# Optimization experiments

Hardware: AMD Instinct MI355X
Metric: run time of the kernel (lower is better)

Reference implementation:

```python
import jax, jax.numpy as jnp
import numpy as np
from jax import lax

B, C, T, D, H, W = 1, 8, 8, 24, 48, 48
KT = 3  # temporal kernel taps (module's time loop == valid forward conv, stride 1, pad 0)
KS = 3  # spatial kernel size
S = 2   # spatial stride of the transposed conv
P = 1   # spatial padding of the transposed conv


def setup_inputs() -> dict:
    key = jax.random.key(0)
    kx, kw = jax.random.split(key)
    x = jax.random.normal(kx, (B, C, T, D, H, W), dtype=jnp.float32)
    # torch layout (out_channels, in_channels, kT, kD, kH, kW); the module assigns the
    # slice weight[:, :, i] directly as ConvTranspose3d.weight, so at runtime dim0 acts
    # as the transpose-conv INPUT-channel dim (works because in_ch == out_ch).
    fan_in = C * KT * KS ** 3
    bound = float(1.0 / np.sqrt(fan_in))
    weight = jax.random.uniform(kw, (C, C, KT, KS, KS, KS), dtype=jnp.float32,
                                minval=-bound, maxval=bound)
    return {"x": x, "weight": weight}


def _convT3d(x5, wt):
    # x5: [N, Cin, D, H, W]; wt: ConvTranspose3d weight laid out [Cin, Cout, kD, kH, kW].
    # Transposed conv == forward conv with spatially flipped kernel, swapped I/O dims,
    # lhs dilation = stride, per-side padding = dil*(k-1) - p.
    rhs = jnp.flip(wt, axis=(2, 3, 4)).transpose(1, 0, 2, 3, 4)  # [Cout, Cin, k, k, k]
    pad = KS - 1 - P
    return lax.conv_general_dilated(
        x5, rhs,
        window_strides=(1, 1, 1),
        padding=[(pad, pad)] * 3,
        lhs_dilation=(S, S, S),
        dimension_numbers=("NCDHW", "OIDHW", "NCDHW"))


def reference(x, weight):
    b, c, t = x.shape[:3]
    t_o = t - (KT - 1)  # temporal valid forward conv: out[f] = sum_i conv_i(x[f + i])
    # fold time into batch so each temporal tap is a single big 3D conv
    xr = x.transpose(0, 2, 1, 3, 4, 5).reshape(b * t, c, *x.shape[3:])
    out = None
    for i in range(KT):  # small fixed loop over kernel taps
        y = _convT3d(xr, weight[:, :, i])                 # [b*t, C, Do, Ho, Wo]
        y = y.reshape(b, t, *y.shape[1:])[:, i:i + t_o]   # frames x[f+i] -> out[f]
        out = y if out is None else out + y
    return out.transpose(0, 2, 1, 3, 4, 5)  # [B, C, t_o, Do, Ho, Wo]
```

## Files before the change

kernel.cpp:

```cpp
#include <hip/hip_runtime.h>


typedef float  f32x4  __attribute__((ext_vector_type(4)));
typedef float  f4a    __attribute__((ext_vector_type(4)));
typedef short  bf16x8 __attribute__((ext_vector_type(8)));
typedef unsigned int u32;
typedef u32    u32x2  __attribute__((ext_vector_type(2)));
typedef u32    u32x4  __attribute__((ext_vector_type(4)));

namespace {
constexpr int T_ = 8, D_ = 24, H_ = 48, W_ = 48;
constexpr int TO = 6, DO_ = 47, HO = 95, WO = 95;
constexpr int XCS = T_ * D_ * H_ * W_;
constexpr int XFS = D_ * H_ * W_;
constexpr int XDS = H_ * W_;
constexpr long OCS = (long)TO * DO_ * HO * WO;
constexpr int OFS = DO_ * HO * WO;
constexpr int ODS = HO * WO;

constexpr int AG[4] = {24, 12, 12, 8};
constexpr int AOFF[4] = {0, 3072, 4608, 6144};
constexpr int NRSTR = 242;

__global__ __launch_bounds__(256) void pack_kernel(const float* __restrict__ w,
                                                   unsigned short* __restrict__ A) {
  const int tid = blockIdx.x * 256 + threadIdx.x;
  const int nthr = gridDim.x * 256;
  const int KR[4] = {192, 96, 96, 48};
  for (int c = 0; c < 4; ++c) {
    const int cnt = AG[c] * 128;
    for (int e = tid; e < cnt; e += nthr) {
      const int j = e & 7, r = (e >> 3) & 15, g = e >> 7;
      const int k = g * 8 + j;
      float v = 0.f;
      if (k < KR[c]) {
        int gg = -1, kd = 1, kh = 1;
        const int cc = j & 1;
        if (c == 0)      { gg = g;               kd = ((j >> 1) & 1) ? 2 : 0; kh = ((j >> 2) & 1) ? 0 : 2; }
        else if (c == 1) { gg = 2 * g + (j >> 2); kd = ((j >> 1) & 1) ? 2 : 0; kh = 1; }
        else if (c == 2) { gg = 2 * g + (j >> 2); kd = 1; kh = ((j >> 1) & 1) ? 0 : 2; }
        else             { gg = 4 * g + (j >> 1); kd = 1; kh = 1; }
        if (gg >= 0 && gg < 24) {
          const int ci = gg / 3, i = gg - 3 * (gg / 3);
          const int co = r & 7;
          int kw = (r < 8) ? (cc == 0 ? 1 : -1) : (cc == 0 ? 2 : 0);
          if (kw >= 0) v = w[ci * 648 + co * 81 + i * 27 + kd * 9 + kh * 3 + kw];
        }
      }
      u32 u = __float_as_uint(v);
      u += 0x7FFFu + ((u >> 16) & 1u);
      A[AOFF[c] + e] = (unsigned short)(u >> 16);
    }
  }
}

__device__ __forceinline__ int rowb(int gg, int dl) {
  const int ci = gg / 3;
  return (ci * 5 + (gg - 3 * ci) + dl) * 6;
}

template<int PD, int PH>
__device__ __forceinline__ void wave_body(
    const u32* __restrict__ lds, const unsigned short* __restrict__ A,
    float* __restrict__ out, int f0, int od, int oh, int ihb, int lane)
{
  constexpr int CLS = (PD && PH) ? 0 : PD ? 1 : PH ? 2 : 3;
  constexpr int NSTEP = (CLS == 0) ? 6 : (CLS == 3) ? 2 : 3;
  const int c15 = lane & 15, q = lane >> 4;
  const int th = ((oh + PH) >> 1) - ihb;

  bf16x8 af[NSTEP];
  {
    const unsigned short* Ap = A + AOFF[CLS] + c15 * 8;
    #pragma unroll
    for (int s = 0; s < NSTEP; ++s)
      af[s] = *reinterpret_cast<const bf16x8*>(Ap + (s * 4 + q) * 128);
  }

  f32x4 acc[3][3];
  #pragma unroll
  for (int dl = 0; dl < 3; ++dl)
    #pragma unroll
    for (int b = 0; b < 3; ++b) acc[dl][b] = {0, 0, 0, 0};

  #pragma unroll
  for (int blk = 0; blk < 3; ++blk) {
    const int n = blk * 16 + c15;
    const u32* col = lds + n * NRSTR;
    #pragma unroll
    for (int s = 0; s < NSTEP; ++s) {
      const int G = s * 4 + q;
      #pragma unroll
      for (int dl = 0; dl < 3; ++dl) {
        u32x4 ue;
        if constexpr (CLS == 0) {
          const u32* b = col + rowb(G, dl) + 2 * th - 2;
          const u32x2 lo = *reinterpret_cast<const u32x2*>(b);
          const u32x2 hi = *reinterpret_cast<const u32x2*>(b + 2);
          ue = u32x4{lo.x, lo.y, hi.x, hi.y};
        } else if constexpr (CLS == 1) {
          const u32* b0 = col + rowb(2 * G, dl) + 2 * th;
          const u32* b1 = col + rowb(2 * G + 1, dl) + 2 * th;
          const u32x2 lo = *reinterpret_cast<const u32x2*>(b0);
          const u32x2 hi = *reinterpret_cast<const u32x2*>(b1);
          ue = u32x4{lo.x, lo.y, hi.x, hi.y};
        } else if constexpr (CLS == 2) {
          const int r0 = rowb(2 * G, dl), r1 = rowb(2 * G + 1, dl);
          ue = u32x4{col[r0 + 2 * th - 1], col[r0 + 2 * th + 1],
                     col[r1 + 2 * th - 1], col[r1 + 2 * th + 1]};
        } else {
          #pragma unroll
          for (int d = 0; d < 4; ++d) {
            int gg = 4 * G + d; gg = (gg > 23) ? 23 : gg;
            ue[d] = col[rowb(gg, dl) + 2 * th + 1];
          }
        }
        acc[dl][blk] = __builtin_amdgcn_mfma_f32_16x16x32_bf16(af[s], __builtin_bit_cast(bf16x8, ue), acc[dl][blk], 0, 0, 0);
      }
    }
  }

  const int isO = (q >= 2);
  const int co0 = (q & 1) * 4;
  #pragma unroll
  for (int dl = 0; dl < 3; ++dl) {
    #pragma unroll
    for (int blk = 0; blk < 3; ++blk) {
      const int ow = blk * 32 + 2 * c15 + isO;
      if (ow < 95) {
        const long ob = (long)(f0 + dl) * OFS + (long)od * ODS + (long)oh * HO + ow;
        #pragma unroll
        for (int j = 0; j < 4; ++j)
          out[(long)(co0 + j) * OCS + ob] = acc[dl][blk][j];
      }
    }
  }
}

constexpr int NBLK = 2 * 24 * 24;

__global__ __launch_bounds__(512) void convt4d_kernel(
    const float* __restrict__ x, const unsigned short* __restrict__ A,
    float* __restrict__ out)
{
  __shared__ u32 lds[48 * NRSTR];

  constexpr int qq = NBLK / 8;
  const int bid = blockIdx.x;
  const int L = (bid & 7) * qq + (bid >> 3);
  const int og = L % 24;
  const int rest = L / 24;
  const int odp = rest % 24, fp = rest / 24;
  const int f0 = 3 * fp;

  const int tid = threadIdx.x;
  const int ihb = og * 2;
  const int idp = odp + 1;

  for (int c = tid; c < 240 * 12; c += 512) {
    const int row = c / 12, ch = c % 12;
    const int ggp = row / 6;
    const int rem = row % 6;
    const int t = rem >> 1, e = rem & 1;
    const int ci = ggp / 5, fi = ggp % 5;
    int plane = idp - e; if (plane > 23) plane = 23;
    int ih = ihb + t; if (ih > 47) ih = 47;
    const float* src = x + ci * XCS + (f0 + fi) * XFS + plane * XDS + ih * W_ + ch * 4;
    const f4a v = *reinterpret_cast<const f4a*>(src);
    const float v4 = (ch == 11) ? 0.f : src[4];
    const u32 b0 = __float_as_uint(v.x), b1 = __float_as_uint(v.y);
    const u32 b2 = __float_as_uint(v.z), b3 = __float_as_uint(v.w);
    const u32 b4 = __float_as_uint(v4);
    u32* dst = lds + (4 * ch) * NRSTR + row;
    dst[0 * NRSTR] = __builtin_amdgcn_perm(b1, b0, 0x07060302u);
    dst[1 * NRSTR] = __builtin_amdgcn_perm(b2, b1, 0x07060302u);
    dst[2 * NRSTR] = __builtin_amdgcn_perm(b3, b2, 0x07060302u);
    dst[3 * NRSTR] = __builtin_amdgcn_perm(b4, b3, 0x07060302u);
  }
  __syncthreads();

  const int w = tid >> 6, lane = tid & 63;
  const int half = w >> 2;
  const int od = 2 * odp + half;
  if (od > 46) return;
  int oh = og * 4 + (w & 3);
  if (oh > 94) oh = 93;
  if (half) {
    if (oh & 1) wave_body<1, 1>(lds, A, out, f0, od, oh, ihb, lane);
    else        wave_body<1, 0>(lds, A, out, f0, od, oh, ihb, lane);
  } else {
    if (oh & 1) wave_body<0, 1>(lds, A, out, f0, od, oh, ihb, lane);
    else        wave_body<0, 0>(lds, A, out, f0, od, oh, ihb, lane);
  }
}
}

extern "C" void kernel_launch(void* const* d_in, const int* in_sizes, int n_in,
                              void* d_out, int out_size, void* d_ws, size_t ws_size,
                              hipStream_t stream) {
  const float* x = (const float*)d_in[0];
  const float* w = (const float*)d_in[1];
  float* out = (float*)d_out;
  unsigned short* A = (unsigned short*)d_ws;
  hipLaunchKernelGGL(pack_kernel, dim3(8), dim3(256), 0, stream, w, A);
  hipLaunchKernelGGL(convt4d_kernel, dim3(NBLK), dim3(512), 0, stream, x, A, out);
}
```

Baseline: 32.88 us.

## Stage input tile via direct global-to-LDS loads, pack bf16 pairs at read time

The input staging loop used to load float4 vectors into registers, build bf16 pairs with perm, and write them transposed into a padded LDS layout. It now copies raw fp32 rows straight into LDS with global_load_lds (16-byte per lane) in row-major order. The bf16 pair packing moves into the MFMA operand gather, where each element becomes two LDS reads plus a perm. Staging gets cheaper, but the inner loop does twice as many LDS reads with a different bank pattern. The unpadded layout may also cause bank conflicts.

```diff
diff --git a/kernel.cpp b/kernel.cpp
--- a/kernel.cpp
+++ b/kernel.cpp
@@ -2,10 +2,8 @@
 
 
 typedef float  f32x4  __attribute__((ext_vector_type(4)));
-typedef float  f4a    __attribute__((ext_vector_type(4)));
 typedef short  bf16x8 __attribute__((ext_vector_type(8)));
 typedef unsigned int u32;
-typedef u32    u32x2  __attribute__((ext_vector_type(2)));
 typedef u32    u32x4  __attribute__((ext_vector_type(4)));
 
 namespace {
@@ -20,7 +18,6 @@
 
 constexpr int AG[4] = {24, 12, 12, 8};
 constexpr int AOFF[4] = {0, 3072, 4608, 6144};
-constexpr int NRSTR = 242;
 
 __global__ __launch_bounds__(256) void pack_kernel(const float* __restrict__ w,
                                                    unsigned short* __restrict__ A) {
@@ -86,7 +83,10 @@
   #pragma unroll
   for (int blk = 0; blk < 3; ++blk) {
     const int n = blk * 16 + c15;
-    const u32* col = lds + n * NRSTR;
+    auto RD = [&](int row) -> u32 {
+      const u32* r = lds + row * 48 + n;
+      return __builtin_amdgcn_perm(r[1], r[0], 0x07060302u);
+    };
     #pragma unroll
     for (int s = 0; s < NSTEP; ++s) {
       const int G = s * 4 + q;
@@ -94,25 +94,21 @@
       for (int dl = 0; dl < 3; ++dl) {
         u32x4 ue;
         if constexpr (CLS == 0) {
-          const u32* b = col + rowb(G, dl) + 2 * th - 2;
-          const u32x2 lo = *reinterpret_cast<const u32x2*>(b);
-          const u32x2 hi = *reinterpret_cast<const u32x2*>(b + 2);
-          ue = u32x4{lo.x, lo.y, hi.x, hi.y};
+          const int b = rowb(G, dl) + 2 * th - 2;
+          ue = u32x4{RD(b), RD(b + 1), RD(b + 2), RD(b + 3)};
         } else if constexpr (CLS == 1) {
-          const u32* b0 = col + rowb(2 * G, dl) + 2 * th;
-          const u32* b1 = col + rowb(2 * G + 1, dl) + 2 * th;
-          const u32x2 lo = *reinterpret_cast<const u32x2*>(b0);
-          const u32x2 hi = *reinterpret_cast<const u32x2*>(b1);
-          ue = u32x4{lo.x, lo.y, hi.x, hi.y};
+          const int b0 = rowb(2 * G, dl) + 2 * th;
+          const int b1 = rowb(2 * G + 1, dl) + 2 * th;
+          ue = u32x4{RD(b0), RD(b0 + 1), RD(b1), RD(b1 + 1)};
         } else if constexpr (CLS == 2) {
           const int r0 = rowb(2 * G, dl), r1 = rowb(2 * G + 1, dl);
-          ue = u32x4{col[r0 + 2 * th - 1], col[r0 + 2 * th + 1],
-                     col[r1 + 2 * th - 1], col[r1 + 2 * th + 1]};
+          ue = u32x4{RD(r0 + 2 * th - 1), RD(r0 + 2 * th + 1),
+                     RD(r1 + 2 * th - 1), RD(r1 + 2 * th + 1)};
         } else {
           #pragma unroll
           for (int d = 0; d < 4; ++d) {
             int gg = 4 * G + d; gg = (gg > 23) ? 23 : gg;
-            ue[d] = col[rowb(gg, dl) + 2 * th + 1];
+            ue[d] = RD(rowb(gg, dl) + 2 * th + 1);
           }
         }
         acc[dl][blk] = __builtin_amdgcn_mfma_f32_16x16x32_bf16(af[s], __builtin_bit_cast(bf16x8, ue), acc[dl][blk], 0, 0, 0);
@@ -143,7 +139,7 @@
     const float* __restrict__ x, const unsigned short* __restrict__ A,
     float* __restrict__ out)
 {
-  __shared__ u32 lds[48 * NRSTR];
+  __shared__ u32 lds[240 * 48 + 16];
 
   constexpr int qq = NBLK / 8;
   const int bid = blockIdx.x;
@@ -157,25 +153,25 @@
   const int ihb = og * 2;
   const int idp = odp + 1;
 
-  for (int c = tid; c < 240 * 12; c += 512) {
-    const int row = c / 12, ch = c % 12;
-    const int ggp = row / 6;
-    const int rem = row % 6;
-    const int t = rem >> 1, e = rem & 1;
-    const int ci = ggp / 5, fi = ggp % 5;
-    int plane = idp - e; if (plane > 23) plane = 23;
-    int ih = ihb + t; if (ih > 47) ih = 47;
-    const float* src = x + ci * XCS + (f0 + fi) * XFS + plane * XDS + ih * W_ + ch * 4;
-    const f4a v = *reinterpret_cast<const f4a*>(src);
-    const float v4 = (ch == 11) ? 0.f : src[4];
-    const u32 b0 = __float_as_uint(v.x), b1 = __float_as_uint(v.y);
-    const u32 b2 = __float_as_uint(v.z), b3 = __float_as_uint(v.w);
-    const u32 b4 = __float_as_uint(v4);
-    u32* dst = lds + (4 * ch) * NRSTR + row;
-    dst[0 * NRSTR] = __builtin_amdgcn_perm(b1, b0, 0x07060302u);
-    dst[1 * NRSTR] = __builtin_amdgcn_perm(b2, b1, 0x07060302u);
-    dst[2 * NRSTR] = __builtin_amdgcn_perm(b3, b2, 0x07060302u);
-    dst[3 * NRSTR] = __builtin_amdgcn_perm(b4, b3, 0x07060302u);
+  {
+    const int wv = tid >> 6, ln = tid & 63;
+    for (int k = wv; k < 45; k += 8) {
+      const int fidx = k * 256 + ln * 4;
+      const int row = fidx / 48;
+      const int off = fidx - row * 48;
+      const int rem = row % 6;
+      const int t = rem >> 1, e = rem & 1;
+      const int ggp = row / 6;
+      const int ci = ggp / 5, fi = ggp - 5 * ci;
+      int plane = idp - e; if (plane > 23) plane = 23;
+      int ih = ihb + t; if (ih > 47) ih = 47;
+      const float* src = x + ci * XCS + (f0 + fi) * XFS + plane * XDS + ih * W_ + off;
+      __builtin_amdgcn_global_load_lds(
+          (const __attribute__((address_space(1))) u32*)src,
+          ((__attribute__((address_space(3))) u32*)lds) + k * 256,
+          16, 0, 0);
+    }
+    if (tid == 0) lds[240 * 48] = 0;
   }
   __syncthreads();
 
```

Result: slower. 39.03 us (+18.7%).
